# Kernel tuning notes

Hardware: AMD Instinct MI355X
Metric: run time of the kernel (lower is better)

The kernel has to match this reference:

```python
import jax, jax.numpy as jnp
import numpy as np

NEG_SLOPE = 0.2
EPS = 1e-6
K = 16


def vec_lna(x, Wf, Wd):
    # x: (B, Cin, 3, ...). Vector-neuron linear + VN-LeakyReLU.
    p = jnp.einsum('oc,bc...->bo...', Wf, x)          # features (B, Cout, 3, ...)
    d = jnp.einsum('oc,bc...->bo...', Wd, x)          # directions (B, Cd, 3, ...), Cd=Cout or 1 (shared)
    dot = jnp.sum(p * d, axis=2, keepdims=True)
    dsq = jnp.sum(d * d, axis=2, keepdims=True)
    p_ref = p - (dot / (dsq + EPS)) * d               # reflect negative part onto hyperplane
    return NEG_SLOPE * p + (1.0 - NEG_SLOPE) * jnp.where(dot >= 0, p, p_ref)


def knn_idx_fn(pts, k):
    # pts: (B, N, 3) -> (B, N, k) indices of k nearest neighbors (incl. self)
    sq = jnp.sum(pts * pts, axis=-1)                  # (B, N)
    d2 = sq[:, :, None] + sq[:, None, :] - 2.0 * jnp.einsum('bnd,bmd->bnm', pts, pts)
    _, idx = jax.lax.top_k(-d2, k)                    # smallest distances
    return idx


def graph_feature(x, idx):
    # x: (B, C, 3, N), idx: (B, N, k) -> (B, 2C, 3, N, k)
    nb = jax.vmap(lambda xb, ib: xb[:, :, ib])(x, idx)  # (B, C, 3, N, k)
    xc = x[..., None]
    return jnp.concatenate([nb - xc, jnp.broadcast_to(xc, nb.shape)], axis=1)


def _winit(key, co, ci):
    return jax.random.normal(key, (co, ci), dtype=jnp.float32) * np.sqrt(2.0 / ci).astype(np.float32)


def setup_inputs() -> dict:
    key = jax.random.key(0)
    ks = jax.random.split(key, 16)
    B, N = 4, 2048
    x = jax.random.normal(ks[0], (B, 3, N), dtype=jnp.float32)
    return {
        'x': x,
        'w1f': _winit(ks[1], 16, 2),   'w1d': _winit(ks[2], 16, 2),
        'w2f': _winit(ks[3], 32, 32),  'w2d': _winit(ks[4], 32, 32),
        'w3f': _winit(ks[5], 64, 64),  'w3d': _winit(ks[6], 64, 64),
        'w4f': _winit(ks[7], 128, 128),'w4d': _winit(ks[8], 128, 128),
        'wcf': _winit(ks[9], 128, 240),'wcd': _winit(ks[10], 1, 240),   # shared nonlinearity -> 1 dir channel
        'wi1f': _winit(ks[11], 128, 256), 'wi1d': _winit(ks[12], 128, 256),
        'wi2f': _winit(ks[13], 256, 128), 'wi2d': _winit(ks[14], 256, 128),
    }


def reference(x, w1f, w1d, w2f, w2d, w3f, w3d, w4f, w4d, wcf, wcd, wi1f, wi1d, wi2f, wi2d):
    # x: (B, 3, N)
    pts = jnp.transpose(x, (0, 2, 1))                 # (B, N, 3)
    idx = knn_idx_fn(pts, K)                          # (B, N, K) -- fixed graph (use_dg=False)
    h = x[:, None]                                    # (B, 1, 3, N)
    h = vec_lna(graph_feature(h, idx), w1f, w1d)
    x1 = h.mean(axis=-1)                              # (B, 16, 3, N)
    h = vec_lna(graph_feature(x1, idx), w2f, w2d)
    x2 = h.mean(axis=-1)                              # (B, 32, 3, N)
    h = vec_lna(graph_feature(x2, idx), w3f, w3d)
    x3 = h.mean(axis=-1)                              # (B, 64, 3, N)
    h = vec_lna(graph_feature(x3, idx), w4f, w4d)
    x4 = h.mean(axis=-1)                              # (B, 128, 3, N)
    xc = vec_lna(jnp.concatenate([x1, x2, x3, x4], axis=1), wcf, wcd)  # (B, 128, 3, N)
    xm = jnp.broadcast_to(xc.mean(axis=-1, keepdims=True), xc.shape)
    xcat = jnp.concatenate([xc, xm], axis=1)          # (B, 256, 3, N)
    x0 = vec_lna(vec_lna(xcat, wi1f, wi1d), wi2f, wi2d)
    inv = jnp.sum(xcat * x0, axis=2)                  # (B, 256, N) rotation-invariant features
    return inv
```

## Files before the change

### kernel.cpp

```cpp
#include <hip/hip_runtime.h>
#include <hip/hip_fp16.h>

#define NPTS  2048
#define BATCH 4
#define NBP   8192
#define MROWS 24576
#define KNN_K 16

typedef short bf16x8 __attribute__((ext_vector_type(8)));
typedef float f32x4  __attribute__((ext_vector_type(4)));

static __device__ __forceinline__ void split_bf16(float a, unsigned short& h, unsigned short& l)
{
    unsigned u = __float_as_uint(a);
    unsigned hr = (u + 0x7FFFu + ((u >> 16) & 1u)) & 0xFFFF0000u;
    h = (unsigned short)(hr >> 16);
    float rem = a - __uint_as_float(hr);
    unsigned v = __float_as_uint(rem);
    l = (unsigned short)((v + 0x7FFFu + ((v >> 16) & 1u)) >> 16);
}

static __device__ __forceinline__ float bf2(unsigned short h, unsigned short l)
{
    return __uint_as_float((unsigned)h << 16) + __uint_as_float((unsigned)l << 16);
}

static __device__ __forceinline__ float lna_scale(float dot, float dsq)
{
    return (dot < 0.f) ? 0.8f * dot * __builtin_amdgcn_rcpf(dsq + 1e-6f) : 0.f;
}

static __device__ __forceinline__ unsigned long long shfl_xor_u64(unsigned long long v, int mask)
{
    unsigned lo = (unsigned)v, hi = (unsigned)(v >> 32);
    lo = (unsigned)__shfl_xor((int)lo, mask, 64);
    hi = (unsigned)__shfl_xor((int)hi, mask, 64);
    return ((unsigned long long)hi << 32) | lo;
}

static __device__ __forceinline__ int xcd_swizzle(int i, int G)
{
    int batch  = (i >> 1) & 3;
    int within = ((i >> 3) << 1) | (i & 1);
    return batch * (G >> 2) + within;
}

static __device__ __forceinline__ float wbig_val(const float* __restrict__ Wf,
                                                 const float* __restrict__ Wd,
                                                 int j, int c, int O, int C)
{
    if (j < 2 * O) {
        int o = j >> 1;
        return (j & 1) ? Wd[o * 2 * C + c] : Wf[o * 2 * C + c];
    }
    int o = (j - 2 * O) >> 1;
    return (j & 1) ? (Wd[o * 2 * C + C + c] - Wd[o * 2 * C + c])
                   : (Wf[o * 2 * C + C + c] - Wf[o * 2 * C + c]);
}

#define PC0 1572864
#define PC1 (PC0 + 4096)
#define PC2 (PC1 + 8192)
#define PC3 (PC2 + 32768)
#define PC4 (PC3 + 49152)
#define PC5 (PC4 + 65536)
#define PC6 (PC5 + 65536)
#define KNN_BLOCKS (NBP / 4)
#define PREP_BLOCKS (PC6 / 256)

__global__ __launch_bounds__(256) void prep_knn_kernel(
    const float* __restrict__ x, int* __restrict__ idx,
    __half* __restrict__ AH, float* __restrict__ AG,
    const float* __restrict__ w1f, const float* __restrict__ w1d,
    const float* __restrict__ w2f, const float* __restrict__ w2d,
    unsigned short* __restrict__ Wb2h, unsigned short* __restrict__ Wb2l,
    const float* __restrict__ w3f, const float* __restrict__ w3d,
    unsigned short* __restrict__ Wb3h, unsigned short* __restrict__ Wb3l,
    const float* __restrict__ w4f, const float* __restrict__ w4d,
    unsigned short* __restrict__ Wb4h, unsigned short* __restrict__ Wb4l,
    const float* __restrict__ wcf, const float* __restrict__ wcd,
    unsigned short* __restrict__ Wch, unsigned short* __restrict__ Wcl,
    const float* __restrict__ wi1f, const float* __restrict__ wi1d,
    unsigned short* __restrict__ Wi1h, unsigned short* __restrict__ Wi1l,
    const float* __restrict__ wi2f, const float* __restrict__ wi2d,
    unsigned short* __restrict__ Wi2h, unsigned short* __restrict__ Wi2l)
{
    __shared__ unsigned ksh[4][64 * 34];
    if (blockIdx.x < KNN_BLOCKS) {
        const int t  = threadIdx.x & 63;
        const int wq = threadIdx.x >> 6;
        const int bn = blockIdx.x * 4 + wq;
        const int b = bn >> 11;
        const int n = bn & (NPTS - 1);
        const float* xb = x + b * 3 * NPTS;
        const float qx = xb[n], qy = xb[NPTS + n], qz = xb[2 * NPTS + n];
        const float sqn = fmaf(qz, qz, fmaf(qy, qy, qx * qx));
        unsigned* ks = &ksh[wq][t * 34];

        unsigned gm[4];
        int ga[4];
#pragma unroll
        for (int g = 0; g < 4; g++) {
            unsigned kk[8];
#pragma unroll
            for (int j = 0; j < 8; j++) {
                const int i = g * 8 + j;
                const int m = (i << 6) + t;
                float mx = xb[m], my = xb[NPTS + m], mz = xb[2 * NPTS + m];
                float sqm = fmaf(mz, mz, fmaf(my, my, mx * mx));
                float dt  = fmaf(qz, mz, fmaf(qy, my, qx * mx));
                float d2  = sqn + sqm - 2.0f * dt;
                unsigned u = __float_as_uint(d2);
                u ^= (u & 0x80000000u) ? 0xFFFFFFFFu : 0x80000000u;
                kk[j] = u;
            }
            *(uint2*)&ks[g * 8 + 0] = make_uint2(kk[0], kk[1]);
            *(uint2*)&ks[g * 8 + 2] = make_uint2(kk[2], kk[3]);
            *(uint2*)&ks[g * 8 + 4] = make_uint2(kk[4], kk[5]);
            *(uint2*)&ks[g * 8 + 6] = make_uint2(kk[6], kk[7]);
            unsigned bg = kk[0];
            int ba = g * 8;
#pragma unroll
            for (int j = 1; j < 8; j++) {
                if (kk[j] < bg) { bg = kk[j]; ba = g * 8 + j; }
            }
            gm[g] = bg; ga[g] = ba;
        }
        unsigned lm = gm[0];
        int il = ga[0];
#pragma unroll
        for (int g = 1; g < 4; g++) if (gm[g] < lm) { lm = gm[g]; il = ga[g]; }

        unsigned long long pk = ((unsigned long long)lm << 32) | (unsigned)((il << 6) | t);
        int res = -1;
        for (int r = 0; r < KNN_K; r++) {
            unsigned long long w = pk;
#pragma unroll
            for (int off = 32; off > 0; off >>= 1) {
                unsigned long long o = shfl_xor_u64(w, off);
                w = (o < w) ? o : w;
            }
            if (t == r) res = (int)(w & 0xFFFFFFFFull);

            if (pk == w) {
                ks[il] = 0xFFFFFFFFu;
                const int g = il >> 3;
                unsigned bg = ks[g * 8];
                int ba = g * 8;
#pragma unroll
                for (int j = 1; j < 8; j++) {
                    unsigned kv = ks[g * 8 + j];
                    if (kv < bg) { bg = kv; ba = g * 8 + j; }
                }
                gm[g] = bg; ga[g] = ba;
                lm = gm[0]; il = ga[0];
#pragma unroll
                for (int g2 = 1; g2 < 4; g2++) if (gm[g2] < lm) { lm = gm[g2]; il = ga[g2]; }
                pk = ((unsigned long long)lm << 32) | (unsigned)((il << 6) | t);
            }
        }
        if (t < KNN_K) idx[bn * KNN_K + t] = res;
        return;
    }

    const int i = (blockIdx.x - KNN_BLOCKS) * 256 + threadIdx.x;
    if (i < PC0) {
        int o = i & 63;
        int row = i >> 6;
        int v = row % 3;
        int gp = row / 3;
        int b = gp >> 11;
        int n = gp & (NPTS - 1);
        float xv = x[(b * 3 + v) * NPTS + n];
        float wv = wbig_val(w1f, w1d, o, 0, 16, 1);
        float val = xv * wv;
        if (o < 32) AH[(size_t)row * 32 + o] = __float2half(val);
        else        AG[(size_t)row * 32 + o - 32] = val;
    } else if (i < PC6) {
        float v = 0.f;
        unsigned short *ph, *pl;
        int ix;
        if (i < PC1) {
            ix = i - PC0;
            int c = ix & 31, j = ix >> 5;
            if (c < 16) v = wbig_val(w2f, w2d, j, c, 32, 16);
            ph = Wb2h; pl = Wb2l;
        } else if (i < PC2) {
            ix = i - PC1;
            int c = ix & 31, j = ix >> 5;
            v = wbig_val(w3f, w3d, j, c, 64, 32);
            ph = Wb3h; pl = Wb3l;
        } else if (i < PC3) {
            ix = i - PC2;
            int c = ix & 63, j = ix >> 6;
            v = wbig_val(w4f, w4d, j, c, 128, 64);
            ph = Wb4h; pl = Wb4l;
        } else if (i < PC4) {
            ix = i - PC3;
            int c = ix & 255, r = ix >> 8;
            if (c < 240) {
                if (r < 128) v = wcf[r * 240 + c];
                else if (r < 129) v = wcd[(r - 128) * 240 + c];
            }
            ph = Wch; pl = Wcl;
        } else if (i < PC5) {
            ix = i - PC4;
            int c = ix & 255, r = ix >> 8;
            if (r < 128) v = wi1f[r * 256 + c];
            else v = wi1d[(r - 128) * 256 + c];
            ph = Wi1h; pl = Wi1l;
        } else {
            ix = i - PC5;
            int c = ix & 127, r = ix >> 7;
            int o = r >> 1;
            v = (r & 1) ? wi2d[o * 128 + c] : wi2f[o * 128 + c];
            ph = Wi2h; pl = Wi2l;
        }
        unsigned short h, l;
        split_bf16(v, h, l);
        ph[ix] = h; pl[ix] = l;
    }
}

template <int OIN, int NF>
__global__ __launch_bounds__(256, 3) void edge_gemm_kernel(
    const __half* __restrict__ AHin, const float* __restrict__ AGin,
    const int* __restrict__ idx,
    unsigned short* __restrict__ X240h, unsigned short* __restrict__ X240l, int ooff,
    const unsigned short* __restrict__ Wh, const unsigned short* __restrict__ Wl,
    __half* __restrict__ OUTA, float* __restrict__ OUTG)
{
    constexpr int PTS = 16;
    constexpr int NC = NF * 64;
    constexpr int twoO = NC / 2;
    constexpr int LDW = 40;
    constexpr int CPT = OIN / 16;
    constexpr int twoOin = 2 * OIN;

    __shared__ unsigned short Xsh[48][32];
    __shared__ unsigned short Xsl[48][32];
    __shared__ unsigned short wbh[NC][LDW];
    __shared__ unsigned short wbl[NC][LDW];
    __shared__ int sIdx[PTS][KNN_K];

    const int lb = xcd_swizzle(blockIdx.x, gridDim.x);
    const int tid = threadIdx.x;

    for (int rr = tid; rr < NC; rr += 256) {
#pragma unroll
        for (int scc = 0; scc < 4; scc++) {
            *(uint4*)&wbh[rr][scc * 8] = *(const uint4*)(Wh + (size_t)rr * 32 + scc * 8);
            *(uint4*)&wbl[rr][scc * 8] = *(const uint4*)(Wl + (size_t)rr * 32 + scc * 8);
        }
    }
    for (int j = tid; j < PTS * KNN_K; j += 256)
        sIdx[j >> 4][j & 15] = idx[(lb * PTS + (j >> 4)) * KNN_K + (j & 15)];
    __syncthreads();

    const int op = tid & 15;
    const int pt = tid >> 4;
    const int gp = lb * PTS + pt;
    const int b = gp >> 11;
    const int rown = gp * 3;
    const int bbase = (b << 11) * 3;

    float cg[3][2 * CPT];
#pragma unroll
    for (int v = 0; v < 3; v++) {
        if constexpr (CPT == 2) {
            float4 c4 = *(const float4*)&AGin[(size_t)(rown + v) * twoOin + 4 * op];
            cg[v][0] = c4.x; cg[v][1] = c4.y; cg[v][2] = c4.z; cg[v][3] = c4.w;
        } else {
            float2 c2 = *(const float2*)&AGin[(size_t)(rown + v) * twoOin + 2 * op];
            cg[v][0] = c2.x; cg[v][1] = c2.y;
        }
    }
    float am[CPT][3];
#pragma unroll
    for (int c0 = 0; c0 < CPT; c0++) { am[c0][0] = 0.f; am[c0][1] = 0.f; am[c0][2] = 0.f; }

#pragma unroll 2
    for (int k = 0; k < KNN_K; k++) {
        const int m = sIdx[pt][k];
        const __half* base = AHin + (size_t)(bbase + m * 3) * twoOin + 2 * CPT * op;
        float e[3][2 * CPT];
#pragma unroll
        for (int v = 0; v < 3; v++) {
            if constexpr (CPT == 2) {
                uint2 u = *(const uint2*)(base + (size_t)v * twoOin);
                float2 x0 = __half22float2(*(__half2*)&u.x);
                float2 x1 = __half22float2(*(__half2*)&u.y);
                e[v][0] = x0.x; e[v][1] = x0.y; e[v][2] = x1.x; e[v][3] = x1.y;
            } else {
                unsigned u = *(const unsigned*)(base + (size_t)v * twoOin);
                float2 x0 = __half22float2(*(__half2*)&u);
                e[v][0] = x0.x; e[v][1] = x0.y;
            }
        }
#pragma unroll
        for (int c0 = 0; c0 < CPT; c0++) {
            float p0 = e[0][2 * c0] + cg[0][2 * c0], d0 = e[0][2 * c0 + 1] + cg[0][2 * c0 + 1];
            float p1 = e[1][2 * c0] + cg[1][2 * c0], d1 = e[1][2 * c0 + 1] + cg[1][2 * c0 + 1];
            float p2 = e[2][2 * c0] + cg[2][2 * c0], d2 = e[2][2 * c0 + 1] + cg[2][2 * c0 + 1];
            float dot = fmaf(p2, d2, fmaf(p1, d1, p0 * d0));
            float dsq = fmaf(d2, d2, fmaf(d1, d1, d0 * d0));
            float s = lna_scale(dot, dsq);
            am[c0][0] += fmaf(-s, d0, p0);
            am[c0][1] += fmaf(-s, d1, p1);
            am[c0][2] += fmaf(-s, d2, p2);
        }
    }

#pragma unroll
    for (int v = 0; v < 3; v++) {
#pragma unroll
        for (int c0 = 0; c0 < CPT; c0++) {
            const int ch = CPT * op + c0;
            unsigned short h, l;
            split_bf16(am[c0][v] * 0.0625f, h, l);
            Xsh[pt * 3 + v][ch] = h;
            Xsl[pt * 3 + v][ch] = l;
            const size_t ob = (size_t)(rown + v) * 256 + ooff + ch;
            X240h[ob] = h; X240l[ob] = l;
        }
        if constexpr (CPT == 1) {
            Xsh[pt * 3 + v][16 + op] = 0;
            Xsl[pt * 3 + v][16 + op] = 0;
        }
    }
    __syncthreads();

    const int lane = tid & 63;
    const int wv = tid >> 6;
    const int mr = lane & 15;
    const int q  = lane >> 4;

    f32x4 acc[3][NF];
#pragma unroll
    for (int a = 0; a < 3; a++)
#pragma unroll
        for (int c = 0; c < NF; c++) acc[a][c] = (f32x4){0.f, 0.f, 0.f, 0.f};

    bf16x8 ah[3], al[3], bh[NF], bl[NF];
#pragma unroll
    for (int mf = 0; mf < 3; mf++) {
        ah[mf] = *(const bf16x8*)&Xsh[mf * 16 + mr][q * 8];
        al[mf] = *(const bf16x8*)&Xsl[mf * 16 + mr][q * 8];
    }
#pragma unroll
    for (int nf = 0; nf < NF; nf++) {
        const int wr = wv * 16 * NF + nf * 16 + mr;
        bh[nf] = *(const bf16x8*)&wbh[wr][q * 8];
        bl[nf] = *(const bf16x8*)&wbl[wr][q * 8];
    }
#pragma unroll
    for (int mf = 0; mf < 3; mf++)
#pragma unroll
        for (int nf = 0; nf < NF; nf++) {
            acc[mf][nf] = __builtin_amdgcn_mfma_f32_16x16x32_bf16(ah[mf], bh[nf], acc[mf][nf], 0, 0, 0);
            acc[mf][nf] = __builtin_amdgcn_mfma_f32_16x16x32_bf16(ah[mf], bl[nf], acc[mf][nf], 0, 0, 0);
            acc[mf][nf] = __builtin_amdgcn_mfma_f32_16x16x32_bf16(al[mf], bh[nf], acc[mf][nf], 0, 0, 0);
        }

    const int rbase = lb * 48;
#pragma unroll
    for (int nf = 0; nf < NF; nf++) {
        const int col = wv * 16 * NF + nf * 16 + mr;
#pragma unroll
        for (int mf = 0; mf < 3; mf++)
#pragma unroll
            for (int i = 0; i < 4; i++) {
                const int row = rbase + mf * 16 + q * 4 + i;
                const float val = acc[mf][nf][i];
                if (col < twoO) OUTA[(size_t)row * twoO + col] = __float2half(val);
                else            OUTG[(size_t)row * twoO + col - twoO] = val;
            }
    }
}

__global__ __launch_bounds__(256) void gemm_mfma(
    const unsigned short* __restrict__ Xh, const unsigned short* __restrict__ Xl,
    int ldx, int xoff,
    const unsigned short* __restrict__ Wh, const unsigned short* __restrict__ Wl,
    float* __restrict__ OUT, int ldo, int Nout, int Kpad,
    __half* __restrict__ OUTA, float* __restrict__ OUTG, int twoO)
{
    __shared__ unsigned short Ws[2][64][56];
    const int tid = threadIdx.x;
    const int bm = blockIdx.x * 256;
    const int bo = blockIdx.y * 64;
    const int lane = tid & 63;
    const int wv = tid >> 6;
    const int mr = lane & 15;
    const int q  = lane >> 4;

    f32x4 acc[4][4];
#pragma unroll
    for (int a = 0; a < 4; a++)
#pragma unroll
        for (int c = 0; c < 4; c++) acc[a][c] = (f32x4){0.f, 0.f, 0.f, 0.f};

    const int wr = tid >> 2;
    const int sc = tid & 3;

    for (int k0 = 0; k0 < Kpad; k0 += 32) {
        {
            const uint4 vh = *(const uint4*)(Wh + (size_t)(bo + wr) * Kpad + k0 + sc * 8);
            const uint4 vl = *(const uint4*)(Wl + (size_t)(bo + wr) * Kpad + k0 + sc * 8);
            *(uint4*)&Ws[0][wr][sc * 8] = vh;
            *(uint4*)&Ws[1][wr][sc * 8] = vl;
        }
        __syncthreads();

        bf16x8 ah[4], al[4], bh[4], bl[4];
#pragma unroll
        for (int mf = 0; mf < 4; mf++) {
            const size_t xrow = (size_t)(bm + wv * 64 + mf * 16 + mr) * ldx + xoff + k0 + q * 8;
            ah[mf] = *(const bf16x8*)(Xh + xrow);
            al[mf] = *(const bf16x8*)(Xl + xrow);
        }
#pragma unroll
        for (int nf = 0; nf < 4; nf++) {
            bh[nf] = *(const bf16x8*)&Ws[0][nf * 16 + mr][q * 8];
            bl[nf] = *(const bf16x8*)&Ws[1][nf * 16 + mr][q * 8];
        }
#pragma unroll
        for (int mf = 0; mf < 4; mf++)
#pragma unroll
            for (int nf = 0; nf < 4; nf++) {
                acc[mf][nf] = __builtin_amdgcn_mfma_f32_16x16x32_bf16(ah[mf], bh[nf], acc[mf][nf], 0, 0, 0);
                acc[mf][nf] = __builtin_amdgcn_mfma_f32_16x16x32_bf16(ah[mf], bl[nf], acc[mf][nf], 0, 0, 0);
                acc[mf][nf] = __builtin_amdgcn_mfma_f32_16x16x32_bf16(al[mf], bh[nf], acc[mf][nf], 0, 0, 0);
            }
        __syncthreads();
    }

    if (OUTA) {
#pragma unroll
        for (int nf = 0; nf < 4; nf++) {
            const int col = bo + nf * 16 + mr;
            if (col < twoO) {
#pragma unroll
                for (int mf = 0; mf < 4; mf++)
#pragma unroll
                    for (int i = 0; i < 4; i++) {
                        const int row = bm + wv * 64 + mf * 16 + q * 4 + i;
                        OUTA[(size_t)row * twoO + col] = __float2half(acc[mf][nf][i]);
                    }
            } else {
#pragma unroll
                for (int mf = 0; mf < 4; mf++)
#pragma unroll
                    for (int i = 0; i < 4; i++) {
                        const int row = bm + wv * 64 + mf * 16 + q * 4 + i;
                        OUTG[(size_t)row * twoO + col - twoO] = acc[mf][nf][i];
                    }
            }
        }
    } else {
#pragma unroll
        for (int nf = 0; nf < 4; nf++) {
            const int col = bo + nf * 16 + mr;
            if (col < Nout) {
#pragma unroll
                for (int mf = 0; mf < 4; mf++)
#pragma unroll
                    for (int i = 0; i < 4; i++) {
                        const int row = bm + wv * 64 + mf * 16 + q * 4 + i;
                        OUT[(size_t)row * ldo + col] = acc[mf][nf][i];
                    }
            }
        }
    }
}

template <int O, int PT>
__global__ __launch_bounds__(256, 6) void edge_kernel(const __half* __restrict__ AH,
                                                      const float* __restrict__ AG,
                                                      const int* __restrict__ idx,
                                                      unsigned short* __restrict__ outh,
                                                      unsigned short* __restrict__ outl,
                                                      int ooff)
{
    constexpr int TP = O / 2;
    constexpr int twoO = 2 * O;
    const int lb = xcd_swizzle(blockIdx.x, gridDim.x);
    const int tid = threadIdx.x;
    const int op = tid % TP;
    const int pt = tid / TP;
    const int gp = lb * PT + pt;
    const int b = gp >> 11;
    __shared__ int sIdx[PT][KNN_K];
    for (int j = tid; j < PT * KNN_K; j += 256)
        sIdx[j >> 4][j & 15] = idx[(lb * PT + (j >> 4)) * KNN_K + (j & 15)];
    __syncthreads();
    const int rown = gp * 3;
    const float4 c0 = *(const float4*)&AG[(size_t)(rown + 0) * twoO + 4 * op];
    const float4 c1 = *(const float4*)&AG[(size_t)(rown + 1) * twoO + 4 * op];
    const float4 c2 = *(const float4*)&AG[(size_t)(rown + 2) * twoO + 4 * op];
    float ax0 = 0.f, ax1 = 0.f, ax2 = 0.f;
    float ay0 = 0.f, ay1 = 0.f, ay2 = 0.f;
    const int bbase = (b << 11) * 3;
#pragma unroll 2
    for (int k = 0; k < KNN_K; k++) {
        int m = sIdx[pt][k];
        const __half* base = AH + (size_t)(bbase + m * 3) * twoO + 4 * op;
        uint2 u0 = *(const uint2*)(base);
        uint2 u1 = *(const uint2*)(base + twoO);
        uint2 u2 = *(const uint2*)(base + 2 * twoO);
        float2 e0 = __half22float2(*(__half2*)&u0.x);
        float2 f0 = __half22float2(*(__half2*)&u0.y);
        float2 e1 = __half22float2(*(__half2*)&u1.x);
        float2 f1 = __half22float2(*(__half2*)&u1.y);
        float2 e2 = __half22float2(*(__half2*)&u2.x);
        float2 f2 = __half22float2(*(__half2*)&u2.y);
        {
            float p0 = e0.x + c0.x, d0 = e0.y + c0.y;
            float p1 = e1.x + c1.x, d1 = e1.y + c1.y;
            float p2 = e2.x + c2.x, d2 = e2.y + c2.y;
            float dot = fmaf(p2, d2, fmaf(p1, d1, p0 * d0));
            float dsq = fmaf(d2, d2, fmaf(d1, d1, d0 * d0));
            float s = lna_scale(dot, dsq);
            ax0 += fmaf(-s, d0, p0);
            ax1 += fmaf(-s, d1, p1);
            ax2 += fmaf(-s, d2, p2);
        }
        {
            float p0 = f0.x + c0.z, d0 = f0.y + c0.w;
            float p1 = f1.x + c1.z, d1 = f1.y + c1.w;
            float p2 = f2.x + c2.z, d2 = f2.y + c2.w;
            float dot = fmaf(p2, d2, fmaf(p1, d1, p0 * d0));
            float dsq = fmaf(d2, d2, fmaf(d1, d1, d0 * d0));
            float s = lna_scale(dot, dsq);
            ay0 += fmaf(-s, d0, p0);
            ay1 += fmaf(-s, d1, p1);
            ay2 += fmaf(-s, d2, p2);
        }
    }
    float rx[3] = { ax0 * 0.0625f, ax1 * 0.0625f, ax2 * 0.0625f };
    float ry[3] = { ay0 * 0.0625f, ay1 * 0.0625f, ay2 * 0.0625f };
#pragma unroll
    for (int v = 0; v < 3; v++) {
        unsigned short hx, lx, hy, ly;
        split_bf16(rx[v], hx, lx);
        split_bf16(ry[v], hy, ly);
        const size_t ob = (size_t)(rown + v) * 256 + ooff + 2 * op;
        *(unsigned*)(outh + ob) = (unsigned)hx | ((unsigned)hy << 16);
        *(unsigned*)(outl + ob) = (unsigned)lx | ((unsigned)ly << 16);
    }
}

#define EW_LDX 136
#define EW_LDT 133
__global__ __launch_bounds__(256, 3) void edge_wc_kernel(
    const __half* __restrict__ AHin, const float* __restrict__ AGin,
    const int* __restrict__ idx,
    const unsigned short* __restrict__ Xh, const unsigned short* __restrict__ Xl,
    const unsigned short* __restrict__ Wh, const unsigned short* __restrict__ Wl,
    unsigned short* __restrict__ oh, unsigned short* __restrict__ ol,
    float* __restrict__ part2)
{
    __shared__ __align__(16) unsigned short x4h[48][EW_LDX];
    __shared__ __align__(16) unsigned short x4l[48][EW_LDX];
    __shared__ __align__(16) float tb[48 * EW_LDT];
    __shared__ int sIdx[16][KNN_K];

    const int lb = xcd_swizzle(blockIdx.x, gridDim.x);
    const int tid = threadIdx.x;

    for (int j = tid; j < 16 * KNN_K; j += 256)
        sIdx[j >> 4][j & 15] = idx[(lb * 16 + (j >> 4)) * KNN_K + (j & 15)];
    __syncthreads();

    {
        const int op = tid & 15;
        const int pt = tid >> 4;
        const int gp = lb * 16 + pt;
        const int b = gp >> 11;
        const int rown = gp * 3;
        const int bbase = (b << 11) * 3;

        float cg[3][16];
#pragma unroll
        for (int v = 0; v < 3; v++) {
            const float* ag = &AGin[(size_t)(rown + v) * 256 + 16 * op];
#pragma unroll
            for (int t = 0; t < 4; t++) {
                float4 c4 = *(const float4*)(ag + 4 * t);
                cg[v][4 * t + 0] = c4.x; cg[v][4 * t + 1] = c4.y;
                cg[v][4 * t + 2] = c4.z; cg[v][4 * t + 3] = c4.w;
            }
        }
        float am[8][3];
#pragma unroll
        for (int c0 = 0; c0 < 8; c0++) { am[c0][0] = 0.f; am[c0][1] = 0.f; am[c0][2] = 0.f; }

        for (int k = 0; k < KNN_K; k++) {
            const int m = sIdx[pt][k];
            const __half* base = AHin + (size_t)(bbase + m * 3) * 256 + 16 * op;
            unsigned uw[3][8];
#pragma unroll
            for (int v = 0; v < 3; v++) {
                uint4 a  = *(const uint4*)(base + (size_t)v * 256);
                uint4 bq = *(const uint4*)(base + (size_t)v * 256 + 8);
                uw[v][0] = a.x;  uw[v][1] = a.y;  uw[v][2] = a.z;  uw[v][3] = a.w;
                uw[v][4] = bq.x; uw[v][5] = bq.y; uw[v][6] = bq.z; uw[v][7] = bq.w;
            }
#pragma unroll
            for (int c0 = 0; c0 < 8; c0++) {
                float2 e0 = __half22float2(*(__half2*)&uw[0][c0]);
                float2 e1 = __half22float2(*(__half2*)&uw[1][c0]);
                float2 e2 = __half22float2(*(__half2*)&uw[2][c0]);
                float p0 = e0.x + cg[0][2 * c0], d0 = e0.y + cg[0][2 * c0 + 1];
                float p1 = e1.x + cg[1][2 * c0], d1 = e1.y + cg[1][2 * c0 + 1];
                float p2 = e2.x + cg[2][2 * c0], d2 = e2.y + cg[2][2 * c0 + 1];
                float dot = fmaf(p2, d2, fmaf(p1, d1, p0 * d0));
                float dsq = fmaf(d2, d2, fmaf(d1, d1, d0 * d0));
                float s = lna_scale(dot, dsq);
                am[c0][0] += fmaf(-s, d0, p0);
                am[c0][1] += fmaf(-s, d1, p1);
                am[c0][2] += fmaf(-s, d2, p2);
            }
        }
#pragma unroll
        for (int v = 0; v < 3; v++)
#pragma unroll
            for (int c0 = 0; c0 < 8; c0++) {
                unsigned short h, l;
                split_bf16(am[c0][v] * 0.0625f, h, l);
                x4h[pt * 3 + v][8 * op + c0] = h;
                x4l[pt * 3 + v][8 * op + c0] = l;
            }
    }
    __syncthreads();

    const int lane = tid & 63;
    const int wv = tid >> 6;
    const int mr = lane & 15;
    const int q  = lane >> 4;
    const int rbase = lb * 48;

    f32x4 acc[3][3];
#pragma unroll
    for (int a = 0; a < 3; a++)
#pragma unroll
        for (int c = 0; c < 3; c++) acc[a][c] = (f32x4){0.f, 0.f, 0.f, 0.f};

    for (int k0 = 0; k0 < 256; k0 += 32) {
        const int kb = k0 + q * 8;
        bf16x8 ah[3], al[3], bh[3], bl[3];
#pragma unroll
        for (int mf = 0; mf < 3; mf++) {
            const int row = mf * 16 + mr;
            if (kb >= 112) {
                if (kb >= 240) {
                    ah[mf] = (bf16x8){0, 0, 0, 0, 0, 0, 0, 0};
                    al[mf] = (bf16x8){0, 0, 0, 0, 0, 0, 0, 0};
                } else {
                    ah[mf] = *(const bf16x8*)&x4h[row][kb - 112];
                    al[mf] = *(const bf16x8*)&x4l[row][kb - 112];
                }
            } else {
                const size_t xr = (size_t)(rbase + row) * 256 + kb;
                ah[mf] = *(const bf16x8*)(Xh + xr);
                al[mf] = *(const bf16x8*)(Xl + xr);
            }
        }
#pragma unroll
        for (int nf = 0; nf < 3; nf++) {
            const size_t wri = (size_t)(wv * 48 + nf * 16 + mr) * 256 + kb;
            bh[nf] = *(const bf16x8*)(Wh + wri);
            bl[nf] = *(const bf16x8*)(Wl + wri);
        }
#pragma unroll
        for (int mf = 0; mf < 3; mf++)
#pragma unroll
            for (int nf = 0; nf < 3; nf++) {
                acc[mf][nf] = __builtin_amdgcn_mfma_f32_16x16x32_bf16(ah[mf], bh[nf], acc[mf][nf], 0, 0, 0);
                acc[mf][nf] = __builtin_amdgcn_mfma_f32_16x16x32_bf16(ah[mf], bl[nf], acc[mf][nf], 0, 0, 0);
                acc[mf][nf] = __builtin_amdgcn_mfma_f32_16x16x32_bf16(al[mf], bh[nf], acc[mf][nf], 0, 0, 0);
            }
    }

#pragma unroll
    for (int mf = 0; mf < 3; mf++)
#pragma unroll
        for (int nf = 0; nf < 3; nf++) {
            const int col = wv * 48 + nf * 16 + mr;
            if (col <= 128) {
#pragma unroll
                for (int i = 0; i < 4; i++)
                    tb[(mf * 16 + q * 4 + i) * EW_LDT + col] = acc[mf][nf][i];
            }
        }
    __syncthreads();

    const int bp0 = lb * 16;
    float vacc[3] = {0.f, 0.f, 0.f};
#pragma unroll
    for (int it = 0; it < 8; it++) {
        const int item = it * 256 + tid;
        const int o = item & 127;
        const int pt = item >> 7;
        float p[3], d[3];
#pragma unroll
        for (int v = 0; v < 3; v++) {
            const int r = pt * 3 + v;
            p[v] = tb[r * EW_LDT + o];
            d[v] = tb[r * EW_LDT + 128];
        }
        float dot = fmaf(p[2], d[2], fmaf(p[1], d[1], p[0] * d[0]));
        float dsq = fmaf(d[2], d[2], fmaf(d[1], d[1], d[0] * d[0]));
        float s = lna_scale(dot, dsq);
#pragma unroll
        for (int v = 0; v < 3; v++) {
            float val = fmaf(-s, d[v], p[v]);
            vacc[v] += val;
            unsigned short h, l;
            split_bf16(val, h, l);
            const size_t ob = ((size_t)(bp0 + pt) * 3 + v) * 128 + o;
            oh[ob] = h; ol[ob] = l;
        }
    }

    __syncthreads();
    tb[tid] = vacc[0]; tb[256 + tid] = vacc[1]; tb[512 + tid] = vacc[2];
    __syncthreads();
    if (tid < 128) {
#pragma unroll
        for (int v = 0; v < 3; v++)
            part2[(size_t)lb * 384 + v * 128 + tid] =
                tb[v * 256 + tid] + tb[v * 256 + tid + 128];
    }
}

__global__ __launch_bounds__(128) void xm_reduce_ym_kernel(
    const float* __restrict__ part2,
    unsigned short* __restrict__ xmh, unsigned short* __restrict__ xml,
    const float* __restrict__ wi1f, const float* __restrict__ wi1d,
    float* __restrict__ ym)
{
    __shared__ float xs[128];
    const int bv = blockIdx.x;
    const int b = bv / 3;
    const int v = bv % 3;
    const int o = threadIdx.x;
    float acc = 0.f;
    for (int i = 0; i < 128; i++)
        acc += part2[(size_t)(b * 128 + i) * 384 + v * 128 + o];
    const float m = acc * (1.f / 2048.f);
    unsigned short h, l;
    split_bf16(m, h, l);
    xmh[bv * 128 + o] = h;
    xml[bv * 128 + o] = l;
    xs[o] = m;
    __syncthreads();
#pragma unroll
    for (int half = 0; half < 2; half++) {
        const int oo = half * 128 + o;
        const float* wrow = (oo < 128) ? (wi1f + (size_t)oo * 256 + 128)
                                       : (wi1d + (size_t)(oo - 128) * 256 + 128);
        float s = 0.f;
        for (int c = 0; c < 128; c++) s = fmaf(wrow[c], xs[c], s);
        ym[(size_t)bv * 256 + oo] = s;
    }
}

#define QI_LDY  136
#define QI_LDT  257
#define QI_LDT2 67
__global__ __launch_bounds__(256, 2) void gemm_ii_kernel(
    const unsigned short* __restrict__ xch, const unsigned short* __restrict__ xcl,
    const unsigned short* __restrict__ W1h, const unsigned short* __restrict__ W1l,
    const unsigned short* __restrict__ W2h, const unsigned short* __restrict__ W2l,
    const unsigned short* __restrict__ xmh, const unsigned short* __restrict__ xml,
    const float* __restrict__ ym,
    float* __restrict__ out)
{
    __shared__ __align__(16) char regA[51456];
    __shared__ __align__(16) unsigned short y1h[48][QI_LDY];
    __shared__ __align__(16) unsigned short y1l[48][QI_LDY];
    unsigned short* wb = (unsigned short*)regA;
    float* tb = (float*)regA;

    const int tid = threadIdx.x;
    const int lane = tid & 63;
    const int wv = tid >> 6;
    const int mr = lane & 15;
    const int q  = lane >> 4;
    const int lb = blockIdx.x;
    const int bm = lb * 48;
    const int bb = (lb * 16) >> 11;

    f32x4 acc[3][4];
#pragma unroll
    for (int a = 0; a < 3; a++)
#pragma unroll
        for (int c = 0; c < 4; c++) acc[a][c] = (f32x4){0.f, 0.f, 0.f, 0.f};

    for (int k0 = 0; k0 < 128; k0 += 32) {
        {
            const int rr = tid;
#pragma unroll
            for (int sc = 0; sc < 4; sc++) {
                *(uint4*)&wb[(size_t)rr * 40 + sc * 8] =
                    *(const uint4*)(W1h + (size_t)rr * 256 + k0 + sc * 8);
                *(uint4*)&wb[(size_t)(256 + rr) * 40 + sc * 8] =
                    *(const uint4*)(W1l + (size_t)rr * 256 + k0 + sc * 8);
            }
        }
        __syncthreads();

        bf16x8 ah[3], al[3], bh[4], bl[4];
#pragma unroll
        for (int mf = 0; mf < 3; mf++) {
            const size_t xr = (size_t)(bm + mf * 16 + mr) * 128 + k0 + q * 8;
            ah[mf] = *(const bf16x8*)(xch + xr);
            al[mf] = *(const bf16x8*)(xcl + xr);
        }
#pragma unroll
        for (int nf = 0; nf < 4; nf++) {
            const int wr = wv * 64 + nf * 16 + mr;
            bh[nf] = *(const bf16x8*)&wb[(size_t)wr * 40 + q * 8];
            bl[nf] = *(const bf16x8*)&wb[(size_t)(256 + wr) * 40 + q * 8];
        }
#pragma unroll
        for (int mf = 0; mf < 3; mf++)
#pragma unroll
            for (int nf = 0; nf < 4; nf++) {
                acc[mf][nf] = __builtin_amdgcn_mfma_f32_16x16x32_bf16(ah[mf], bh[nf], acc[mf][nf], 0, 0, 0);
                acc[mf][nf] = __builtin_amdgcn_mfma_f32_16x16x32_bf16(ah[mf], bl[nf], acc[mf][nf], 0, 0, 0);
                acc[mf][nf] = __builtin_amdgcn_mfma_f32_16x16x32_bf16(al[mf], bh[nf], acc[mf][nf], 0, 0, 0);
            }
        __syncthreads();
    }

#pragma unroll
    for (int mf = 0; mf < 3; mf++)
#pragma unroll
        for (int nf = 0; nf < 4; nf++)
#pragma unroll
            for (int i = 0; i < 4; i++)
                tb[(size_t)(mf * 16 + q * 4 + i) * QI_LDT + wv * 64 + nf * 16 + mr] = acc[mf][nf][i];
    __syncthreads();

    {
        const int oo = tid & 127;
        float ymp[3], ymd[3];
#pragma unroll
        for (int v = 0; v < 3; v++) {
            ymp[v] = ym[(size_t)(bb * 3 + v) * 256 + oo];
            ymd[v] = ym[(size_t)(bb * 3 + v) * 256 + 128 + oo];
        }
#pragma unroll
        for (int it = 0; it < 8; it++) {
            const int item = it * 256 + tid;
            const int o = item & 127;
            const int pt = item >> 7;
            float p[3], d[3];
#pragma unroll
            for (int v = 0; v < 3; v++) {
                const int r = pt * 3 + v;
                p[v] = tb[(size_t)r * QI_LDT + o] + ymp[v];
                d[v] = tb[(size_t)r * QI_LDT + 128 + o] + ymd[v];
            }
            float dot = fmaf(p[2], d[2], fmaf(p[1], d[1], p[0] * d[0]));
            float dsq = fmaf(d[2], d[2], fmaf(d[1], d[1], d[0] * d[0]));
            float s = lna_scale(dot, dsq);
#pragma unroll
            for (int v = 0; v < 3; v++) {
                unsigned short h, l;
                split_bf16(fmaf(-s, d[v], p[v]), h, l);
                y1h[pt * 3 + v][o] = h;
                y1l[pt * 3 + v][o] = l;
            }
        }
    }
    __syncthreads();

    f32x4 acc2[3][8];
#pragma unroll
    for (int a = 0; a < 3; a++)
#pragma unroll
        for (int c = 0; c < 8; c++) acc2[a][c] = (f32x4){0.f, 0.f, 0.f, 0.f};

    for (int k0 = 0; k0 < 128; k0 += 32) {
        bf16x8 ah[3], al[3];
#pragma unroll
        for (int mf = 0; mf < 3; mf++) {
            ah[mf] = *(const bf16x8*)&y1h[mf * 16 + mr][k0 + q * 8];
            al[mf] = *(const bf16x8*)&y1l[mf * 16 + mr][k0 + q * 8];
        }
#pragma unroll
        for (int nf = 0; nf < 8; nf++) {
            const size_t wi = (size_t)(wv * 128 + nf * 16 + mr) * 128 + k0 + q * 8;
            const bf16x8 bh = *(const bf16x8*)(W2h + wi);
            const bf16x8 bl = *(const bf16x8*)(W2l + wi);
#pragma unroll
            for (int mf = 0; mf < 3; mf++) {
                acc2[mf][nf] = __builtin_amdgcn_mfma_f32_16x16x32_bf16(ah[mf], bh, acc2[mf][nf], 0, 0, 0);
                acc2[mf][nf] = __builtin_amdgcn_mfma_f32_16x16x32_bf16(ah[mf], bl, acc2[mf][nf], 0, 0, 0);
                acc2[mf][nf] = __builtin_amdgcn_mfma_f32_16x16x32_bf16(al[mf], bh, acc2[mf][nf], 0, 0, 0);
            }
        }
    }

    float* wt = tb + wv * (48 * QI_LDT2);
#pragma unroll
    for (int hf = 0; hf < 2; hf++) {
        __syncthreads();
#pragma unroll
        for (int mf = 0; mf < 3; mf++)
#pragma unroll
            for (int nf2 = 0; nf2 < 4; nf2++)
#pragma unroll
                for (int i = 0; i < 4; i++)
                    wt[(mf * 16 + q * 4 + i) * QI_LDT2 + nf2 * 16 + mr] = acc2[mf][hf * 4 + nf2][i];
#pragma unroll
        for (int j = 0; j < 8; j++) {
            const int item = j * 64 + lane;
            const int ol = item & 31;
            const int pt = item >> 5;
            const int og = wv * 64 + hf * 32 + ol;
            const int gp = lb * 16 + pt;
            float p[3], d[3], xc[3];
#pragma unroll
            for (int v = 0; v < 3; v++) {
                p[v] = wt[(3 * pt + v) * QI_LDT2 + 2 * ol];
                d[v] = wt[(3 * pt + v) * QI_LDT2 + 2 * ol + 1];
                if (og < 128) {
                    const size_t ix = (size_t)(gp * 3 + v) * 128 + og;
                    xc[v] = bf2(xch[ix], xcl[ix]);
                } else {
                    const size_t ix = (size_t)(bb * 3 + v) * 128 + og - 128;
                    xc[v] = bf2(xmh[ix], xml[ix]);
                }
            }
            float dot = fmaf(p[2], d[2], fmaf(p[1], d[1], p[0] * d[0]));
            float dsq = fmaf(d[2], d[2], fmaf(d[1], d[1], d[0] * d[0]));
            float s = lna_scale(dot, dsq);
            float inv = 0.f;
#pragma unroll
            for (int v = 0; v < 3; v++)
                inv = fmaf(xc[v], fmaf(-s, d[v], p[v]), inv);
            out[((size_t)bb * 256 + og) * NPTS + (gp & (NPTS - 1))] = inv;
        }
    }
}

extern "C" void kernel_launch(void* const* d_in, const int* in_sizes, int n_in,
                              void* d_out, int out_size, void* d_ws, size_t ws_size,
                              hipStream_t stream)
{
    const float* x    = (const float*)d_in[0];
    const float* w1f  = (const float*)d_in[1];
    const float* w1d  = (const float*)d_in[2];
    const float* w2f  = (const float*)d_in[3];
    const float* w2d  = (const float*)d_in[4];
    const float* w3f  = (const float*)d_in[5];
    const float* w3d  = (const float*)d_in[6];
    const float* w4f  = (const float*)d_in[7];
    const float* w4d  = (const float*)d_in[8];
    const float* wcf  = (const float*)d_in[9];
    const float* wcd  = (const float*)d_in[10];
    const float* wi1f = (const float*)d_in[11];
    const float* wi1d = (const float*)d_in[12];
    const float* wi2f = (const float*)d_in[13];
    const float* wi2d = (const float*)d_in[14];
    float* out = (float*)d_out;

    float* F = (float*)d_ws;
    size_t off = 0;
    float* AG = F + off;                          off += (size_t)MROWS * 512;
    __half* AH = (__half*)(F + off);              off += (size_t)MROWS * 128;
    __half* AH2 = (__half*)(F + off);             off += (size_t)MROWS * 128;
    unsigned short* X240h = (unsigned short*)(F + off); off += (size_t)MROWS * 128;
    unsigned short* X240l = (unsigned short*)(F + off); off += (size_t)MROWS * 128;
    unsigned short* xc2h  = (unsigned short*)(F + off); off += (size_t)MROWS * 64;
    unsigned short* xc2l  = (unsigned short*)(F + off); off += (size_t)MROWS * 64;
    unsigned short* Wb2h = (unsigned short*)(F + off); off += 2048;
    unsigned short* Wb2l = (unsigned short*)(F + off); off += 2048;
    unsigned short* Wb3h = (unsigned short*)(F + off); off += 4096;
    unsigned short* Wb3l = (unsigned short*)(F + off); off += 4096;
    unsigned short* Wb4h = (unsigned short*)(F + off); off += 16384;
    unsigned short* Wb4l = (unsigned short*)(F + off); off += 16384;
    unsigned short* Wch  = (unsigned short*)(F + off); off += 24576;
    unsigned short* Wcl  = (unsigned short*)(F + off); off += 24576;
    unsigned short* Wi1h = (unsigned short*)(F + off); off += 32768;
    unsigned short* Wi1l = (unsigned short*)(F + off); off += 32768;
    unsigned short* Wi2h = (unsigned short*)(F + off); off += 32768;
    unsigned short* Wi2l = (unsigned short*)(F + off); off += 32768;
    float* part2 = F + off;                       off += (size_t)512 * 384;
    float* ym    = F + off;                       off += 12 * 256;
    unsigned short* xmph = (unsigned short*)(F + off); off += 768;
    unsigned short* xmpl = (unsigned short*)(F + off); off += 768;
    int* idx    = (int*)(F + off);                off += NBP * KNN_K;
    float* AG2 = AG + (size_t)MROWS * 256;

    prep_knn_kernel<<<KNN_BLOCKS + PREP_BLOCKS, 256, 0, stream>>>(
        x, idx, AH, AG, w1f, w1d,
        w2f, w2d, Wb2h, Wb2l, w3f, w3d, Wb3h, Wb3l, w4f, w4d, Wb4h, Wb4l,
        wcf, wcd, Wch, Wcl, wi1f, wi1d, Wi1h, Wi1l, wi2f, wi2d, Wi2h, Wi2l);

    const int GM = MROWS / 256;

    edge_gemm_kernel<16, 2><<<NBP / 16, 256, 0, stream>>>(
        AH, AG, idx, X240h, X240l, 0, Wb2h, Wb2l, AH2, AG2);
    edge_gemm_kernel<32, 4><<<NBP / 16, 256, 0, stream>>>(
        AH2, AG2, idx, X240h, X240l, 16, Wb3h, Wb3l, AH, AG);
    edge_kernel<64, 8><<<NBP / 8, 256, 0, stream>>>(AH, AG, idx, X240h, X240l, 48);
    gemm_mfma<<<dim3(GM, 8), 256, 0, stream>>>(X240h, X240l, 256, 48, Wb4h, Wb4l, nullptr, 0, 512, 64, AH2, AG2, 256);

    edge_wc_kernel<<<NBP / 16, 256, 0, stream>>>(AH2, AG2, idx, X240h, X240l,
                                                 Wch, Wcl, xc2h, xc2l, part2);

    xm_reduce_ym_kernel<<<BATCH * 3, 128, 0, stream>>>(part2, xmph, xmpl, wi1f, wi1d, ym);

    gemm_ii_kernel<<<MROWS / 48, 256, 0, stream>>>(xc2h, xc2l, Wi1h, Wi1l,
                                                   Wi2h, Wi2l, xmph, xmpl, ym, out);

    (void)in_sizes; (void)n_in; (void)out_size; (void)ws_size;
}
```

Baseline: 264.3 us.

## Store weights in MFMA fragment order, alias LDS, prefetch W1 tiles into registers

```diff
diff --git a/kernel.cpp b/kernel.cpp
--- a/kernel.cpp
+++ b/kernel.cpp
@@ -56,6 +56,11 @@
     int o = (j - 2 * O) >> 1;
     return (j & 1) ? (Wd[o * 2 * C + C + c] - Wd[o * 2 * C + c])
                    : (Wf[o * 2 * C + C + c] - Wf[o * 2 * C + c]);
+}
+
+static __device__ __forceinline__ int frag_ix(int r, int c, int RB)
+{
+    return (((c >> 5) * RB + (r >> 4)) * 64 + ((c >> 3) & 3) * 16 + (r & 15)) * 8 + (c & 7);
 }
 
 #define PC0 1572864
@@ -203,6 +208,7 @@
                 else if (r < 129) v = wcd[(r - 128) * 240 + c];
             }
             ph = Wch; pl = Wcl;
+            ix = frag_ix(r, c, 12);
         } else if (i < PC5) {
             ix = i - PC4;
             int c = ix & 255, r = ix >> 8;
@@ -215,6 +221,7 @@
             int o = r >> 1;
             v = (r & 1) ? wi2d[o * 128 + c] : wi2f[o * 128 + c];
             ph = Wi2h; pl = Wi2l;
+            ix = frag_ix(r, c, 32);
         }
         unsigned short h, l;
         split_bf16(v, h, l);
@@ -552,7 +559,7 @@
 
 #define EW_LDX 136
 #define EW_LDT 133
-__global__ __launch_bounds__(256, 3) void edge_wc_kernel(
+__global__ __launch_bounds__(256, 4) void edge_wc_kernel(
     const __half* __restrict__ AHin, const float* __restrict__ AGin,
     const int* __restrict__ idx,
     const unsigned short* __restrict__ Xh, const unsigned short* __restrict__ Xl,
@@ -560,9 +567,10 @@
     unsigned short* __restrict__ oh, unsigned short* __restrict__ ol,
     float* __restrict__ part2)
 {
-    __shared__ __align__(16) unsigned short x4h[48][EW_LDX];
-    __shared__ __align__(16) unsigned short x4l[48][EW_LDX];
-    __shared__ __align__(16) float tb[48 * EW_LDT];
+    __shared__ __align__(16) char smem[48 * EW_LDX * 2 * 2];
+    unsigned short (*x4h)[EW_LDX] = (unsigned short (*)[EW_LDX])smem;
+    unsigned short (*x4l)[EW_LDX] = (unsigned short (*)[EW_LDX])(smem + 48 * EW_LDX * 2);
+    float* tb = (float*)smem;
     __shared__ int sIdx[16][KNN_K];
 
     const int lb = xcd_swizzle(blockIdx.x, gridDim.x);
@@ -668,7 +676,7 @@
         }
 #pragma unroll
         for (int nf = 0; nf < 3; nf++) {
-            const size_t wri = (size_t)(wv * 48 + nf * 16 + mr) * 256 + kb;
+            const size_t wri = (size_t)((((k0 >> 5) * 12) + wv * 3 + nf) * 64 + lane) * 8;
             bh[nf] = *(const bf16x8*)(Wh + wri);
             bl[nf] = *(const bf16x8*)(Wl + wri);
         }
@@ -681,6 +689,7 @@
                 acc[mf][nf] = __builtin_amdgcn_mfma_f32_16x16x32_bf16(al[mf], bh[nf], acc[mf][nf], 0, 0, 0);
             }
     }
+    __syncthreads();
 
 #pragma unroll
     for (int mf = 0; mf < 3; mf++)
@@ -798,18 +807,28 @@
 #pragma unroll
         for (int c = 0; c < 4; c++) acc[a][c] = (f32x4){0.f, 0.f, 0.f, 0.f};
 
+    uint4 pwh[4], pwl[4];
+#pragma unroll
+    for (int sc = 0; sc < 4; sc++) {
+        pwh[sc] = *(const uint4*)(W1h + (size_t)tid * 256 + sc * 8);
+        pwl[sc] = *(const uint4*)(W1l + (size_t)tid * 256 + sc * 8);
+    }
+
     for (int k0 = 0; k0 < 128; k0 += 32) {
-        {
-            const int rr = tid;
+#pragma unroll
+        for (int sc = 0; sc < 4; sc++) {
+            *(uint4*)&wb[(size_t)tid * 40 + sc * 8] = pwh[sc];
+            *(uint4*)&wb[(size_t)(256 + tid) * 40 + sc * 8] = pwl[sc];
+        }
+        __syncthreads();
+
+        if (k0 < 96) {
 #pragma unroll
             for (int sc = 0; sc < 4; sc++) {
-                *(uint4*)&wb[(size_t)rr * 40 + sc * 8] =
-                    *(const uint4*)(W1h + (size_t)rr * 256 + k0 + sc * 8);
-                *(uint4*)&wb[(size_t)(256 + rr) * 40 + sc * 8] =
-                    *(const uint4*)(W1l + (size_t)rr * 256 + k0 + sc * 8);
-            }
-        }
-        __syncthreads();
+                pwh[sc] = *(const uint4*)(W1h + (size_t)tid * 256 + k0 + 32 + sc * 8);
+                pwl[sc] = *(const uint4*)(W1l + (size_t)tid * 256 + k0 + 32 + sc * 8);
+            }
+        }
 
         bf16x8 ah[3], al[3], bh[4], bl[4];
 #pragma unroll
@@ -884,6 +903,7 @@
 #pragma unroll
         for (int c = 0; c < 8; c++) acc2[a][c] = (f32x4){0.f, 0.f, 0.f, 0.f};
 
+#pragma unroll
     for (int k0 = 0; k0 < 128; k0 += 32) {
         bf16x8 ah[3], al[3];
 #pragma unroll
@@ -893,7 +913,7 @@
         }
 #pragma unroll
         for (int nf = 0; nf < 8; nf++) {
-            const size_t wi = (size_t)(wv * 128 + nf * 16 + mr) * 128 + k0 + q * 8;
+            const size_t wi = (size_t)((((k0 >> 5) * 32) + wv * 8 + nf) * 64 + lane) * 8;
             const bf16x8 bh = *(const bf16x8*)(W2h + wi);
             const bf16x8 bl = *(const bf16x8*)(W2l + wi);
 #pragma unroll
```

Measured after the change: 267.9 us. No clear change (+1.4%).
